# Optimization experiments

Measured on AMD Instinct MI355X. Metric: run time of the kernel, lower is better.

The kernel has to match this reference:

```python
import jax, jax.numpy as jnp
import numpy as np

B, L, H, ED, NCONV = 64, 2048, 128, 4, 3
N = B * L


def gat(x, src, dst, edge_attr, W, a_s, a_d, We, a_e, b, self_loops):
    """PyG GATConv, heads=1, concat=True, negative_slope=0.2, fill_value='mean'."""
    n = x.shape[0]
    h = x @ W                              # [N,H]
    a_src = h @ a_s                        # [N]
    a_dst = h @ a_d                        # [N]
    alpha = a_src[src] + a_dst[dst] + (edge_attr @ We) @ a_e  # [E]
    if self_loops:
        ones = jnp.ones(src.shape[0], x.dtype)
        deg = jax.ops.segment_sum(ones, dst, num_segments=n)
        mean_attr = jax.ops.segment_sum(edge_attr, dst, num_segments=n) / jnp.maximum(deg, 1.0)[:, None]
        loop_alpha = a_src + a_dst + (mean_attr @ We) @ a_e
        idx = jnp.arange(n, dtype=src.dtype)
        src = jnp.concatenate([src, idx])
        dst = jnp.concatenate([dst, idx])
        alpha = jnp.concatenate([alpha, loop_alpha])
    alpha = jax.nn.leaky_relu(alpha, 0.2)
    m = jax.ops.segment_max(alpha, dst, num_segments=n)
    ex = jnp.exp(alpha - m[dst])
    den = jax.ops.segment_sum(ex, dst, num_segments=n)
    coef = ex / jnp.maximum(den, 1e-16)[dst]
    return jax.ops.segment_sum(coef[:, None] * h[src], dst, num_segments=n) + b


def setup_inputs() -> dict:
    key = jax.random.key(0)
    ks = iter(jax.random.split(key, 32))
    # binary trees: per graph, node k>0 has parent (k-1)//2; edge child->parent (to_up)
    local = np.arange(1, L)
    parent = (local - 1) // 2
    offs = (np.arange(B) * L)[:, None]
    src = jnp.asarray((local[None, :] + offs).ravel(), dtype=jnp.int32)
    dst = jnp.asarray((parent[None, :] + offs).ravel(), dtype=jnp.int32)
    E = src.shape[0]
    s = 0.1
    inp = {
        "x": jax.random.normal(next(ks), (N,), jnp.float32),
        "src": src,
        "dst": dst,
        "edge_attr": jax.random.normal(next(ks), (E, ED), jnp.float32),
        "up_W0": jax.random.normal(next(ks), (1, H)) * s,
        "up_W": jax.random.normal(next(ks), (NCONV - 1, H, H)) * s,
        "up_att_src": jax.random.normal(next(ks), (NCONV, H)) * s,
        "up_att_dst": jax.random.normal(next(ks), (NCONV, H)) * s,
        "up_We": jax.random.normal(next(ks), (NCONV, ED, H)) * s,
        "up_att_edge": jax.random.normal(next(ks), (NCONV, H)) * s,
        "up_b": jax.random.normal(next(ks), (NCONV, H)) * s,
        "down_W": jax.random.normal(next(ks), (NCONV - 1, H, H)) * s,
        "down_att_src": jax.random.normal(next(ks), (NCONV - 1, H)) * s,
        "down_att_dst": jax.random.normal(next(ks), (NCONV - 1, H)) * s,
        "down_We": jax.random.normal(next(ks), (NCONV - 1, ED, H)) * s,
        "down_att_edge": jax.random.normal(next(ks), (NCONV - 1, H)) * s,
        "down_b": jax.random.normal(next(ks), (NCONV - 1, H)) * s,
        "lin_W": jax.random.normal(next(ks), (NCONV - 1, H, H)) * s,
        "lin_b": jax.random.normal(next(ks), (NCONV - 1, H)) * s,
        "lin_last_W": jax.random.normal(next(ks), (H, 1)) * s,
        "lin_last_b": jax.random.normal(next(ks), (1,)) * s,
    }
    return inp


def reference(x, src, dst, edge_attr, up_W0, up_W, up_att_src, up_att_dst, up_We,
              up_att_edge, up_b, down_W, down_att_src, down_att_dst, down_We,
              down_att_edge, down_b, lin_W, lin_b, lin_last_W, lin_last_b):
    h = x[:, None]                                            # flat_c.view(-1,1)
    # upward pass: toup GATConvs (with self loops) + relu
    for i in range(NCONV):
        W = up_W0 if i == 0 else up_W[i - 1]
        h = jax.nn.relu(gat(h, src, dst, edge_attr, W, up_att_src[i], up_att_dst[i],
                            up_We[i], up_att_edge[i], up_b[i], True))
    x_up = h
    # downward pass uses reversed edges, no self loops; replicates original's
    # indexing bug (todown[0] used twice, todown[-1] never used)
    src_d, dst_d = dst, src
    x_down = jax.nn.relu(gat(x_up, src_d, dst_d, edge_attr, down_W[0], down_att_src[0],
                             down_att_dst[0], down_We[0], down_att_edge[0], down_b[0], False))
    xx = x_down + x_up
    for i in range(NCONV - 1):
        xx = jax.nn.relu(xx @ lin_W[i] + lin_b[i])
        x_down = jax.nn.relu(gat(xx, src_d, dst_d, edge_attr, down_W[i], down_att_src[i],
                                 down_att_dst[i], down_We[i], down_att_edge[i], down_b[i], False))
        xx = x_down + x_up
    final_emb = xx
    out_nodes = xx @ lin_last_W + lin_last_b                  # [N,1]
    batch_out = out_nodes.reshape(B, L)                       # all graphs are max_len
    batch_emb = final_emb.reshape(B, L, H)
    out = batch_out - batch_out[:, :1]                        # subtract root node
    return out, batch_emb
```

## Files before the change

kernel.cpp:

```cpp
#include <hip/hip_runtime.h>
#include <hip/hip_bf16.h>
#include <cstdint>
#include <cstddef>

typedef unsigned short u16;
typedef short bf16x8 __attribute__((ext_vector_type(8)));
typedef float f32x4 __attribute__((ext_vector_type(4)));

#define Bn 64
#define Ln 2048
#define Hn 128
#define EDn 4
#define Nn (Bn*Ln)

#define CV_W0    0
#define CV_WUP   128
#define CV_AS    32896
#define CV_AD    33280
#define CV_WE    33664
#define CV_AE    35200
#define CV_BUP   35584
#define CV_WD    35968
#define CV_BD    68736
#define CV_WL    68992
#define CV_BL    101760
#define CV_WLAST 102016
#define CV_TOTAL 102144

__device__ __forceinline__ float b2f(u16 u) {
  union { float f; unsigned int i; } v; v.i = ((unsigned int)u) << 16; return v.f;
}
__device__ __forceinline__ u16 f2b(float f) {
  __hip_bfloat16 h = __float2bfloat16(f);
  union { __hip_bfloat16 h; u16 u; } v; v.h = h; return v.u;
}
__device__ __forceinline__ float lrelu(float v) { return v >= 0.f ? v : 0.2f * v; }
__device__ __forceinline__ float wave_sum(float r) {
  #pragma unroll
  for (int off = 32; off > 0; off >>= 1) r += __shfl_xor(r, off, 64);
  return r;
}
__device__ __forceinline__ float ld_in(const void* p, size_t i, int f) {
  return f ? b2f(((const u16*)p)[i]) : ((const float*)p)[i];
}
__device__ __forceinline__ u16* Cbase(void* dout, int f) {
  return f ? ((u16*)dout + Nn) : (u16*)((float*)dout + Nn);
}
__device__ __forceinline__ float lo16(unsigned v) { return b2f((u16)(v & 0xFFFF)); }
__device__ __forceinline__ float hi16(unsigned v) { return b2f((u16)(v >> 16)); }

__device__ __forceinline__ void gload_lds16(const void* g, void* l) {
  __builtin_amdgcn_global_load_lds(
      (const __attribute__((address_space(1))) void*)g,
      (__attribute__((address_space(3))) void*)l, 16, 0, 0);
}

__device__ __forceinline__ int xcd_remap(int bid, int nwg) {
  return (bid & 7) * (nwg >> 3) + (bid >> 3);
}

__global__ void detect_kernel(const u16* __restrict__ x, int* __restrict__ flag) {
  int lane = threadIdx.x;
  u16 u = x[lane];
  int e = (u >> 7) & 0xFF;
  bool good = (e >= 100 && e <= 140) || ((u & 0x7FFF) == 0);
  unsigned long long m = __ballot(good);
  if (lane == 0) *flag = (__popcll(m) >= 56) ? 1 : 0;
}

struct CvtArgs { const void* src[12]; int off[12]; int tr[12]; };
__global__ void cvt_kernel(CvtArgs a, const int* __restrict__ flagp, u16* __restrict__ dst) {
  int f = *flagp;
  int i = blockIdx.x * 256 + threadIdx.x;
  if (i >= CV_TOTAL) return;
  int s = 0;
  #pragma unroll
  for (int k = 1; k < 12; ++k) s = (i >= a.off[k]) ? k : s;
  int j = i - a.off[s];
  int sj = j;
  if (a.tr[s]) {
    int mat = j >> 14, jm = j & 16383;
    int r = jm >> 7, c = jm & 127;
    int us = c >> 3, sub = c & 7;
    int u = us ^ (r & 15);
    int k = u * 8 + sub;
    sj = (mat << 14) + k * 128 + r;
  }
  dst[i] = f ? ((const u16*)a.src[s])[sj] : f2b(((const float*)a.src[s])[sj]);
}

__global__ void up0_kernel(const void* __restrict__ x, const void* __restrict__ edge_attr,
                           const u16* __restrict__ W0, const u16* __restrict__ att_s,
                           const u16* __restrict__ att_d, const u16* __restrict__ We0,
                           const u16* __restrict__ ae0, const u16* __restrict__ b0,
                           u16* __restrict__ y, const int* __restrict__ flagp) {
  __shared__ float P[6];
  __shared__ float comb[64];
  __shared__ float W0s[Hn];
  __shared__ float b0s[Hn];
  int f = *flagp;
  int t = threadIdx.x;
  int lane = t & 63, w = t >> 6;
  if (w < 2) {
    const u16* vb = (w == 0) ? att_s : att_d;
    float r = b2f(W0[lane]) * b2f(vb[lane]) + b2f(W0[lane+64]) * b2f(vb[lane+64]);
    r = wave_sum(r);
    if (lane == 0) P[w] = r;
  } else {
    int e0 = (w - 2) * 2;
    float a0 = b2f(ae0[lane]), a1 = b2f(ae0[lane+64]);
    float r0 = b2f(We0[e0*Hn+lane])*a0     + b2f(We0[e0*Hn+lane+64])*a1;
    float r1 = b2f(We0[(e0+1)*Hn+lane])*a0 + b2f(We0[(e0+1)*Hn+lane+64])*a1;
    r0 = wave_sum(r0); r1 = wave_sum(r1);
    if (lane == 0) { P[2+e0] = r0; P[3+e0] = r1; }
  }
  if (t < Hn) { W0s[t] = b2f(W0[t]); b0s[t] = b2f(b0[t]); }
  __syncthreads();
  int base = xcd_remap(blockIdx.x, gridDim.x) * 64;
  if (t < 64) {
    int n = base + t;
    int local = n & (Ln - 1);
    int nb = n >> 11;
    int root = n - local;
    float S0 = P[0], D0 = P[1];
    float w0 = P[2], w1 = P[3], w2 = P[4], w3 = P[5];
    float xp = ld_in(x, n, f);
    float ad_p = D0 * xp;
    int c1l = 2*local + 1, c2l = 2*local + 2;
    int deg = (c1l < Ln ? 1 : 0) + (c2l < Ln ? 1 : 0);
    float e1 = 0.f, e2 = 0.f, xc1 = 0.f, xc2 = 0.f, sc1 = 0.f, sc2 = 0.f;
    if (deg >= 1) {
      xc1 = ld_in(x, root + c1l, f);
      size_t ei = ((size_t)nb*(Ln-1) + (c1l-1))*EDn;
      e1 = ld_in(edge_attr, ei+0, f)*w0 + ld_in(edge_attr, ei+1, f)*w1
         + ld_in(edge_attr, ei+2, f)*w2 + ld_in(edge_attr, ei+3, f)*w3;
      sc1 = lrelu(S0*xc1 + ad_p + e1);
    }
    if (deg == 2) {
      xc2 = ld_in(x, root + c2l, f);
      size_t ei = ((size_t)nb*(Ln-1) + (c2l-1))*EDn;
      e2 = ld_in(edge_attr, ei+0, f)*w0 + ld_in(edge_attr, ei+1, f)*w1
         + ld_in(edge_attr, ei+2, f)*w2 + ld_in(edge_attr, ei+3, f)*w3;
      sc2 = lrelu(S0*xc2 + ad_p + e2);
    }
    float mean_e = deg ? (e1 + e2) / (float)deg : 0.f;
    float ss = lrelu(S0*xp + ad_p + mean_e);
    float m = ss;
    if (deg >= 1) m = fmaxf(m, sc1);
    if (deg == 2) m = fmaxf(m, sc2);
    float es  = __expf(ss - m);
    float ec1 = (deg >= 1) ? __expf(sc1 - m) : 0.f;
    float ec2 = (deg == 2) ? __expf(sc2 - m) : 0.f;
    float den = es + ec1 + ec2;
    comb[t] = (es*xp + ec1*xc1 + ec2*xc2) / den;
  }
  __syncthreads();
  u16* out = y + (size_t)base * Hn;
  for (int i = t; i < 64*Hn/4; i += 256) {
    int row = i >> 5;
    int col = (i & 31) * 4;
    float c = comb[row];
    ushort4 st;
    st.x = f2b(fmaxf(c*W0s[col+0] + b0s[col+0], 0.f));
    st.y = f2b(fmaxf(c*W0s[col+1] + b0s[col+1], 0.f));
    st.z = f2b(fmaxf(c*W0s[col+2] + b0s[col+2], 0.f));
    st.w = f2b(fmaxf(c*W0s[col+3] + b0s[col+3], 0.f));
    *(ushort4*)&out[(size_t)i*4] = st;
  }
}

template<int GATHER, int EPI, int ASAD>
__global__ __launch_bounds__(256, 4) void gemm_k(
                       const u16* __restrict__ Xp, const u16* __restrict__ Wt,
                       const u16* __restrict__ bias, const u16* __restrict__ Uarr,
                       u16* __restrict__ outp, void* __restrict__ dout,
                       const int* __restrict__ flagp, int x_is_C, int out_mode,
                       float2* __restrict__ asad, const u16* __restrict__ avs,
                       const u16* __restrict__ avd, float* __restrict__ nodesp) {
  __shared__ u16 Ws[Hn*Hn];
  int f = *flagp;
  const u16* X = x_is_C ? Cbase(dout, f) : Xp;
  int t = threadIdx.x;
  int lane = t & 63, w = t >> 6;
  int m = lane & 15, q = lane >> 4;
  int row0 = xcd_remap(blockIdx.x, gridDim.x) * 128;
  int wbase = row0 + w*32;
  #pragma unroll
  for (int i = 0; i < 8; ++i)
    gload_lds16(Wt + (size_t)(i*256 + t)*8, &Ws[(size_t)(i*256 + (t & ~63))*8]);
  uint4 xf[2][4];
  #pragma unroll
  for (int rt = 0; rt < 2; ++rt) {
    int R = wbase + rt*16 + m;
    bool zero = false;
    const uint4* src;
    if (GATHER) {
      int local = R & (Ln - 1);
      if (local == 0) { zero = true; src = (const uint4*)X; }
      else src = (const uint4*)(X + (size_t)((R - local) + ((local - 1) >> 1))*Hn);
    } else {
      src = (const uint4*)(X + (size_t)R*Hn);
    }
    #pragma unroll
    for (int ki = 0; ki < 4; ++ki) {
      uint4 v = src[ki*4 + q];
      if (zero) { v.x = 0; v.y = 0; v.z = 0; v.w = 0; }
      xf[rt][ki] = v;
    }
  }
  __syncthreads();
  u16* Cb = Cbase(dout, f);
  float* emf = (float*)dout + Nn;
  u16* od = (out_mode == 0) ? outp : (out_mode == 1 ? Cb : (u16*)dout + Nn);
  float asv[2] = {0.f, 0.f}, adv[2] = {0.f, 0.f};
  #pragma unroll
  for (int cb = 0; cb < 2; ++cb) {
    f32x4 acc[2][4];
    #pragma unroll
    for (int rt = 0; rt < 2; ++rt)
      #pragma unroll
      for (int c4 = 0; c4 < 4; ++c4) acc[rt][c4] = (f32x4){0.f, 0.f, 0.f, 0.f};
    #pragma unroll
    for (int ki = 0; ki < 4; ++ki) {
      #pragma unroll
      for (int c4 = 0; c4 < 4; ++c4) {
        int ct = cb*4 + c4;
        bf16x8 wf = *(bf16x8*)&Ws[((ct*16 + m)*16 + ((ki*4 + q) ^ m))*8];
        #pragma unroll
        for (int rt = 0; rt < 2; ++rt)
          acc[rt][c4] = __builtin_amdgcn_mfma_f32_16x16x32_bf16(
                          wf, *(bf16x8*)&xf[rt][ki], acc[rt][c4], 0, 0, 0);
      }
    }
    #pragma unroll
    for (int rt = 0; rt < 2; ++rt) {
      int R = wbase + rt*16 + m;
      #pragma unroll
      for (int c4 = 0; c4 < 4; ++c4) {
        int ct = cb*4 + c4;
        int c0 = ct*16 + q*4;
        float o[4];
        #pragma unroll
        for (int r = 0; r < 4; ++r) o[r] = acc[rt][c4][r];
        if (ASAD == 1) {
          ushort4 sv = *(const ushort4*)&avs[c0];
          ushort4 dv = *(const ushort4*)&avd[c0];
          asv[rt] += o[0]*b2f(sv.x) + o[1]*b2f(sv.y) + o[2]*b2f(sv.z) + o[3]*b2f(sv.w);
          adv[rt] += o[0]*b2f(dv.x) + o[1]*b2f(dv.y) + o[2]*b2f(dv.z) + o[3]*b2f(dv.w);
        }
        if (EPI >= 1) {
          ushort4 bv = *(const ushort4*)&bias[c0];
          o[0] = fmaxf(o[0] + b2f(bv.x), 0.f); o[1] = fmaxf(o[1] + b2f(bv.y), 0.f);
          o[2] = fmaxf(o[2] + b2f(bv.z), 0.f); o[3] = fmaxf(o[3] + b2f(bv.w), 0.f);
        }
        if (EPI == 2) {
          ushort4 uv = *(const ushort4*)&Uarr[(size_t)R*Hn + c0];
          o[0] += b2f(uv.x); o[1] += b2f(uv.y); o[2] += b2f(uv.z); o[3] += b2f(uv.w);
        }
        if (ASAD == 2) {
          ushort4 sv = *(const ushort4*)&avs[c0];
          asv[rt] += o[0]*b2f(sv.x) + o[1]*b2f(sv.y) + o[2]*b2f(sv.z) + o[3]*b2f(sv.w);
        }
        if (out_mode == 2 && !f) {
          float4 fv; fv.x = o[0]; fv.y = o[1]; fv.z = o[2]; fv.w = o[3];
          *(float4*)&emf[(size_t)R*Hn + c0] = fv;
        } else {
          ushort4 st; st.x = f2b(o[0]); st.y = f2b(o[1]); st.z = f2b(o[2]); st.w = f2b(o[3]);
          *(ushort4*)&od[(size_t)R*Hn + c0] = st;
        }
      }
    }
  }
  #pragma unroll
  for (int rt = 0; rt < 2; ++rt) {
    int R = wbase + rt*16 + m;
    if (ASAD == 1) {
      float as_ = asv[rt], ad_ = adv[rt];
      as_ += __shfl_xor(as_, 16, 64); as_ += __shfl_xor(as_, 32, 64);
      ad_ += __shfl_xor(ad_, 16, 64); ad_ += __shfl_xor(ad_, 32, 64);
      if (q == 0) { float2 v; v.x = as_; v.y = ad_; asad[R] = v; }
    }
    if (ASAD == 2) {
      float as_ = asv[rt];
      as_ += __shfl_xor(as_, 16, 64); as_ += __shfl_xor(as_, 32, 64);
      if (q == 0) nodesp[R] = as_;
    }
  }
}

__global__ __launch_bounds__(256, 4) void gemm_blend_k(
                       const u16* __restrict__ Wt, const float2* __restrict__ coef,
                       const u16* __restrict__ bias_up, u16* __restrict__ outp,
                       void* __restrict__ dout, const int* __restrict__ flagp,
                       float2* __restrict__ asad, const u16* __restrict__ avs,
                       const u16* __restrict__ avd) {
  __shared__ u16 Ws[Hn*Hn];
  int f = *flagp;
  const u16* h = Cbase(dout, f);
  int t = threadIdx.x;
  int lane = t & 63, w = t >> 6;
  int m = lane & 15, q = lane >> 4;
  int row0 = xcd_remap(blockIdx.x, gridDim.x) * 128;
  int wbase = row0 + w*32;
  #pragma unroll
  for (int i = 0; i < 8; ++i)
    gload_lds16(Wt + (size_t)(i*256 + t)*8, &Ws[(size_t)(i*256 + (t & ~63))*8]);
  uint4 xf[2][4];
  #pragma unroll
  for (int rt = 0; rt < 2; ++rt) {
    int R = wbase + rt*16 + m;
    int local = R & (Ln - 1);
    int root = R - local;
    int c1l = 2*local + 1, c2l = 2*local + 2;
    int r1 = (c1l < Ln) ? root + c1l : R;
    int r2 = (c2l < Ln) ? root + c2l : R;
    float2 cf = coef[R];
    float es = 1.f - cf.x - cf.y;
    const uint4* hp = (const uint4*)(h + (size_t)R*Hn);
    const uint4* h1 = (const uint4*)(h + (size_t)r1*Hn);
    const uint4* h2 = (const uint4*)(h + (size_t)r2*Hn);
    #pragma unroll
    for (int ki = 0; ki < 4; ++ki) {
      int u = ki*4 + q;
      uint4 a = hp[u], b = h1[u], c = h2[u];
      uint4 bv = ((const uint4*)bias_up)[u];
      uint4 st;
      #pragma unroll
      for (int i = 0; i < 4; ++i) {
        unsigned av = ((unsigned*)&a)[i], b1v = ((unsigned*)&b)[i];
        unsigned b2v = ((unsigned*)&c)[i], bbv = ((unsigned*)&bv)[i];
        float o0 = es*lo16(av) + cf.x*lo16(b1v) + cf.y*lo16(b2v) + lo16(bbv);
        float o1 = es*hi16(av) + cf.x*hi16(b1v) + cf.y*hi16(b2v) + hi16(bbv);
        ((unsigned*)&st)[i] = (unsigned)f2b(fmaxf(o0, 0.f))
                            | ((unsigned)f2b(fmaxf(o1, 0.f)) << 16);
      }
      xf[rt][ki] = st;
    }
  }
  __syncthreads();
  float asv[2] = {0.f, 0.f}, adv[2] = {0.f, 0.f};
  #pragma unroll
  for (int cb = 0; cb < 2; ++cb) {
    f32x4 acc[2][4];
    #pragma unroll
    for (int rt = 0; rt < 2; ++rt)
      #pragma unroll
      for (int c4 = 0; c4 < 4; ++c4) acc[rt][c4] = (f32x4){0.f, 0.f, 0.f, 0.f};
    #pragma unroll
    for (int ki = 0; ki < 4; ++ki) {
      #pragma unroll
      for (int c4 = 0; c4 < 4; ++c4) {
        int ct = cb*4 + c4;
        bf16x8 wf = *(bf16x8*)&Ws[((ct*16 + m)*16 + ((ki*4 + q) ^ m))*8];
        #pragma unroll
        for (int rt = 0; rt < 2; ++rt)
          acc[rt][c4] = __builtin_amdgcn_mfma_f32_16x16x32_bf16(
                          wf, *(bf16x8*)&xf[rt][ki], acc[rt][c4], 0, 0, 0);
      }
    }
    #pragma unroll
    for (int rt = 0; rt < 2; ++rt) {
      int R = wbase + rt*16 + m;
      #pragma unroll
      for (int c4 = 0; c4 < 4; ++c4) {
        int ct = cb*4 + c4;
        int c0 = ct*16 + q*4;
        float o0 = acc[rt][c4][0], o1 = acc[rt][c4][1];
        float o2 = acc[rt][c4][2], o3 = acc[rt][c4][3];
        ushort4 sv = *(const ushort4*)&avs[c0];
        ushort4 dv = *(const ushort4*)&avd[c0];
        asv[rt] += o0*b2f(sv.x) + o1*b2f(sv.y) + o2*b2f(sv.z) + o3*b2f(sv.w);
        adv[rt] += o0*b2f(dv.x) + o1*b2f(dv.y) + o2*b2f(dv.z) + o3*b2f(dv.w);
        ushort4 st; st.x = f2b(o0); st.y = f2b(o1); st.z = f2b(o2); st.w = f2b(o3);
        *(ushort4*)&outp[(size_t)R*Hn + c0] = st;
      }
    }
  }
  #pragma unroll
  for (int rt = 0; rt < 2; ++rt) {
    int R = wbase + rt*16 + m;
    float as_ = asv[rt], ad_ = adv[rt];
    as_ += __shfl_xor(as_, 16, 64); as_ += __shfl_xor(as_, 32, 64);
    ad_ += __shfl_xor(ad_, 16, 64); ad_ += __shfl_xor(ad_, 32, 64);
    if (q == 0) { float2 v; v.x = as_; v.y = ad_; asad[R] = v; }
  }
}

__global__ __launch_bounds__(512, 4) void fused_down_lin_k(
                       const u16* __restrict__ Xp, const u16* __restrict__ Wdt,
                       const u16* __restrict__ bd, const u16* __restrict__ Uarr,
                       const u16* __restrict__ Wlt, const u16* __restrict__ bl,
                       u16* __restrict__ outp) {
  __shared__ u16 Ws[Hn*Hn];
  __shared__ u16 XX[128*Hn];
  int t = threadIdx.x;
  int lane = t & 63, w = t >> 6;
  int m = lane & 15, q = lane >> 4;
  int row0 = xcd_remap(blockIdx.x, gridDim.x) * 128;
  int R = row0 + w*16 + m;
  int rl = w*16 + m;
  #pragma unroll
  for (int i = 0; i < 4; ++i)
    gload_lds16(Wdt + (size_t)(i*512 + t)*8, &Ws[(size_t)(i*512 + (t & ~63))*8]);
  uint4 xf[4];
  {
    int local = R & (Ln - 1);
    bool zero = (local == 0);
    const uint4* src = zero ? (const uint4*)Xp
                     : (const uint4*)(Xp + (size_t)((R - local) + ((local - 1) >> 1))*Hn);
    #pragma unroll
    for (int ki = 0; ki < 4; ++ki) {
      uint4 v = src[ki*4 + q];
      if (zero) { v.x = 0; v.y = 0; v.z = 0; v.w = 0; }
      xf[ki] = v;
    }
  }
  __syncthreads();
  f32x4 acc[8];
  #pragma unroll
  for (int ct = 0; ct < 8; ++ct) acc[ct] = (f32x4){0.f, 0.f, 0.f, 0.f};
  #pragma unroll
  for (int ki = 0; ki < 4; ++ki) {
    #pragma unroll
    for (int ct = 0; ct < 8; ++ct) {
      bf16x8 wf = *(bf16x8*)&Ws[((ct*16 + m)*16 + ((ki*4 + q) ^ m))*8];
      acc[ct] = __builtin_amdgcn_mfma_f32_16x16x32_bf16(
                    wf, *(bf16x8*)&xf[ki], acc[ct], 0, 0, 0);
    }
  }
  __syncthreads();
  #pragma unroll
  for (int i = 0; i < 4; ++i)
    gload_lds16(Wlt + (size_t)(i*512 + t)*8, &Ws[(size_t)(i*512 + (t & ~63))*8]);
  #pragma unroll
  for (int ct = 0; ct < 8; ++ct) {
    int c0 = ct*16 + q*4;
    ushort4 bv = *(const ushort4*)&bd[c0];
    ushort4 uv = *(const ushort4*)&Uarr[(size_t)R*Hn + c0];
    float o0 = fmaxf(acc[ct][0] + b2f(bv.x), 0.f) + b2f(uv.x);
    float o1 = fmaxf(acc[ct][1] + b2f(bv.y), 0.f) + b2f(uv.y);
    float o2 = fmaxf(acc[ct][2] + b2f(bv.z), 0.f) + b2f(uv.z);
    float o3 = fmaxf(acc[ct][3] + b2f(bv.w), 0.f) + b2f(uv.w);
    int uu = (2*ct + (q >> 1)) ^ m;
    uint2 pk;
    pk.x = (unsigned)f2b(o0) | ((unsigned)f2b(o1) << 16);
    pk.y = (unsigned)f2b(o2) | ((unsigned)f2b(o3) << 16);
    *(uint2*)&XX[rl*Hn + uu*8 + (q & 1)*4] = pk;
  }
  __syncthreads();
  f32x4 acc2[8];
  #pragma unroll
  for (int ct = 0; ct < 8; ++ct) acc2[ct] = (f32x4){0.f, 0.f, 0.f, 0.f};
  #pragma unroll
  for (int ki = 0; ki < 4; ++ki) {
    #pragma unroll
    for (int ct = 0; ct < 8; ++ct) {
      bf16x8 wf = *(bf16x8*)&Ws[((ct*16 + m)*16 + ((ki*4 + q) ^ m))*8];
      bf16x8 xb = *(bf16x8*)&XX[rl*Hn + (((ki*4 + q) ^ m))*8];
      acc2[ct] = __builtin_amdgcn_mfma_f32_16x16x32_bf16(wf, xb, acc2[ct], 0, 0, 0);
    }
  }
  #pragma unroll
  for (int ct = 0; ct < 8; ++ct) {
    int c0 = ct*16 + q*4;
    ushort4 bv = *(const ushort4*)&bl[c0];
    ushort4 st;
    st.x = f2b(fmaxf(acc2[ct][0] + b2f(bv.x), 0.f));
    st.y = f2b(fmaxf(acc2[ct][1] + b2f(bv.y), 0.f));
    st.z = f2b(fmaxf(acc2[ct][2] + b2f(bv.z), 0.f));
    st.w = f2b(fmaxf(acc2[ct][3] + b2f(bv.w), 0.f));
    *(ushort4*)&outp[(size_t)R*Hn + c0] = st;
  }
}

__global__ void coef_kernel(const void* __restrict__ edge_attr,
                            const u16* __restrict__ We, const u16* __restrict__ ae,
                            const float2* __restrict__ asad, float2* __restrict__ coef,
                            const int* __restrict__ flagp) {
  __shared__ float P[4];
  int f = *flagp;
  int t = threadIdx.x;
  int lane = t & 63, w = t >> 6;
  {
    unsigned av = *(const unsigned*)&ae[2*lane];
    unsigned wv = *(const unsigned*)&We[w*Hn + 2*lane];
    float r = wave_sum(lo16(wv)*lo16(av) + hi16(wv)*hi16(av));
    if (lane == 0) P[w] = r;
  }
  __syncthreads();
  int p = xcd_remap(blockIdx.x, gridDim.x) * 256 + t;
  int local = p & (Ln - 1);
  int root = p - local;
  int nb = p >> 11;
  int c1l = 2*local + 1, c2l = 2*local + 2;
  int deg = (c1l < Ln ? 1 : 0) + (c2l < Ln ? 1 : 0);
  float2 aa = asad[p];
  float w0 = P[0], w1 = P[1], w2 = P[2], w3 = P[3];
  float e1 = 0.f, e2 = 0.f, sc1 = 0.f, sc2 = 0.f;
  if (deg >= 1) {
    size_t ei = ((size_t)nb*(Ln-1) + (c1l-1))*EDn;
    if (f) {
      ushort4 v = *(const ushort4*)((const u16*)edge_attr + ei);
      e1 = b2f(v.x)*w0 + b2f(v.y)*w1 + b2f(v.z)*w2 + b2f(v.w)*w3;
      if (deg == 2) {
        ushort4 v2 = *(const ushort4*)((const u16*)edge_attr + ei + EDn);
        e2 = b2f(v2.x)*w0 + b2f(v2.y)*w1 + b2f(v2.z)*w2 + b2f(v2.w)*w3;
      }
    } else {
      float4 v = *(const float4*)((const float*)edge_attr + ei);
      e1 = v.x*w0 + v.y*w1 + v.z*w2 + v.w*w3;
      if (deg == 2) {
        float4 v2 = *(const float4*)((const float*)edge_attr + ei + EDn);
        e2 = v2.x*w0 + v2.y*w1 + v2.z*w2 + v2.w*w3;
      }
    }
    sc1 = lrelu(asad[root + c1l].x + aa.y + e1);
    if (deg == 2) sc2 = lrelu(asad[root + c2l].x + aa.y + e2);
  }
  float mean_e = deg ? (e1 + e2) / (float)deg : 0.f;
  float ss = lrelu(aa.x + aa.y + mean_e);
  float m = ss;
  if (deg >= 1) m = fmaxf(m, sc1);
  if (deg == 2) m = fmaxf(m, sc2);
  float es  = __expf(ss - m);
  float ec1 = (deg >= 1) ? __expf(sc1 - m) : 0.f;
  float ec2 = (deg == 2) ? __expf(sc2 - m) : 0.f;
  float inv = 1.f / (es + ec1 + ec2);
  float2 cf; cf.x = ec1 * inv; cf.y = ec2 * inv;
  coef[p] = cf;
}

__global__ void blend_kernel(const u16* __restrict__ h, const float2* __restrict__ coef,
                             const u16* __restrict__ bias, u16* __restrict__ y) {
  int t = threadIdx.x;
  int g = t & 15;
  int p = xcd_remap(blockIdx.x, gridDim.x) * 16 + (t >> 4);
  int local = p & (Ln - 1);
  int root = p - local;
  int c1l = 2*local + 1, c2l = 2*local + 2;
  int deg = (c1l < Ln ? 1 : 0) + (c2l < Ln ? 1 : 0);
  float2 cf = coef[p];
  float es = 1.f - cf.x - cf.y;
  int off = g * 8;
  uint4 hp = *(const uint4*)&h[(size_t)p*Hn + off];
  uint4 h1 = {0,0,0,0}, h2 = {0,0,0,0};
  if (deg >= 1) h1 = *(const uint4*)&h[(size_t)(root + c1l)*Hn + off];
  if (deg == 2) h2 = *(const uint4*)&h[(size_t)(root + c2l)*Hn + off];
  uint4 bv = *(const uint4*)&bias[off];
  uint4 st;
  #pragma unroll
  for (int i = 0; i < 4; ++i) {
    unsigned a = ((unsigned*)&hp)[i], b1 = ((unsigned*)&h1)[i];
    unsigned b2 = ((unsigned*)&h2)[i], bb = ((unsigned*)&bv)[i];
    float o0 = es*lo16(a) + cf.x*lo16(b1) + cf.y*lo16(b2) + lo16(bb);
    float o1 = es*hi16(a) + cf.x*hi16(b1) + cf.y*hi16(b2) + hi16(bb);
    ((unsigned*)&st)[i] = (unsigned)f2b(fmaxf(o0, 0.f)) | ((unsigned)f2b(fmaxf(o1, 0.f)) << 16);
  }
  *(uint4*)&y[(size_t)p*Hn + off] = st;
}

__global__ void score_kernel(const float* __restrict__ nodes, void* __restrict__ dout,
                             const int* __restrict__ flagp) {
  int f = *flagp;
  int n = xcd_remap(blockIdx.x, gridDim.x) * 256 + threadIdx.x;
  float v = nodes[n] - nodes[n & ~(Ln - 1)];
  if (f) ((u16*)dout)[n] = f2b(v);
  else   ((float*)dout)[n] = v;
}

extern "C" void kernel_launch(void* const* d_in, const int* in_sizes, int n_in,
                              void* d_out, int out_size, void* d_ws, size_t ws_size,
                              hipStream_t stream) {
  const void* x         = d_in[0];
  const void* edge_attr = d_in[3];

  u16* Ubuf = (u16*)d_ws;
  u16* Abuf = Ubuf + (size_t)Nn*Hn;
  u16* Bbuf = Abuf + (size_t)Nn*Hn;
  u16* cvt  = Bbuf + (size_t)Nn*Hn;
  float2* asad = (float2*)(cvt + CV_TOTAL);
  float2* coef = asad + Nn;
  float* nodes = (float*)(coef + Nn);
  int* flag = (int*)(nodes + Nn);

  detect_kernel<<<1, 64, 0, stream>>>((const u16*)d_in[0], flag);

  CvtArgs ca;
  ca.src[0]  = d_in[4];  ca.off[0]  = CV_W0;    ca.tr[0]  = 0;
  ca.src[1]  = d_in[5];  ca.off[1]  = CV_WUP;   ca.tr[1]  = 1;
  ca.src[2]  = d_in[6];  ca.off[2]  = CV_AS;    ca.tr[2]  = 0;
  ca.src[3]  = d_in[7];  ca.off[3]  = CV_AD;    ca.tr[3]  = 0;
  ca.src[4]  = d_in[8];  ca.off[4]  = CV_WE;    ca.tr[4]  = 0;
  ca.src[5]  = d_in[9];  ca.off[5]  = CV_AE;    ca.tr[5]  = 0;
  ca.src[6]  = d_in[10]; ca.off[6]  = CV_BUP;   ca.tr[6]  = 0;
  ca.src[7]  = d_in[11]; ca.off[7]  = CV_WD;    ca.tr[7]  = 1;
  ca.src[8]  = d_in[16]; ca.off[8]  = CV_BD;    ca.tr[8]  = 0;
  ca.src[9]  = d_in[17]; ca.off[9]  = CV_WL;    ca.tr[9]  = 1;
  ca.src[10] = d_in[18]; ca.off[10] = CV_BL;    ca.tr[10] = 0;
  ca.src[11] = d_in[19]; ca.off[11] = CV_WLAST; ca.tr[11] = 0;
  cvt_kernel<<<(CV_TOTAL + 255)/256, 256, 0, stream>>>(ca, flag, cvt);

  up0_kernel<<<Nn/64, 256, 0, stream>>>(x, edge_attr, cvt+CV_W0, cvt+CV_AS, cvt+CV_AD,
                                        cvt+CV_WE, cvt+CV_AE, cvt+CV_BUP, Abuf, flag);
  gemm_k<0,0,1><<<Nn/128, 256, 0, stream>>>(Abuf, cvt+CV_WUP, nullptr, nullptr,
                                         nullptr, d_out, flag, 0, 1,
                                         asad, cvt+CV_AS+Hn, cvt+CV_AD+Hn, nullptr);
  coef_kernel<<<Nn/256, 256, 0, stream>>>(edge_attr, cvt+CV_WE+EDn*Hn, cvt+CV_AE+Hn,
                                          asad, coef, flag);
  gemm_blend_k<<<Nn/128, 256, 0, stream>>>(cvt+CV_WUP+Hn*Hn, coef, cvt+CV_BUP+Hn,
                                           Bbuf, d_out, flag,
                                           asad, cvt+CV_AS+2*Hn, cvt+CV_AD+2*Hn);
  coef_kernel<<<Nn/256, 256, 0, stream>>>(edge_attr, cvt+CV_WE+2*EDn*Hn, cvt+CV_AE+2*Hn,
                                          asad, coef, flag);
  blend_kernel<<<Nn/16, 256, 0, stream>>>(Bbuf, coef, cvt+CV_BUP+2*Hn, Ubuf);

  fused_down_lin_k<<<Nn/128, 512, 0, stream>>>(Ubuf, cvt+CV_WD, cvt+CV_BD, Ubuf,
                                               cvt+CV_WL, cvt+CV_BL, Abuf);
  fused_down_lin_k<<<Nn/128, 512, 0, stream>>>(Abuf, cvt+CV_WD, cvt+CV_BD, Ubuf,
                                               cvt+CV_WL+Hn*Hn, cvt+CV_BL+Hn, Bbuf);
  gemm_k<1,2,2><<<Nn/128, 256, 0, stream>>>(Bbuf, cvt+CV_WD+Hn*Hn, cvt+CV_BD+Hn, Ubuf,
                                         nullptr, d_out, flag, 0, 2,
                                         nullptr, cvt+CV_WLAST, nullptr, nodes);

  score_kernel<<<Nn/256, 256, 0, stream>>>(nodes, d_out, flag);
}
```

Baseline: 277.5 us.

## Fuse attention coefficient computation into blend kernels and double rows per gemm block

The two coef_kernel launches are removed; each consumer (gemm_blend_k, blend_kernel) recomputes softmax coefficients inline from asad and edge_attr, with the small edge-weight dot products precomputed once by a new prep_kernel. gemm_k now processes 256 rows per block, loading the weight tile into LDS once and prefetching the second row tile while the first is computed, with launch bounds lowered to 3. A separate asad2 buffer avoids a read/write hazard on asad. This removes launches and the coef round-trip, at the cost of redundant coefficient math per thread, higher register pressure and half as many gemm blocks.

```diff
diff --git a/kernel.cpp b/kernel.cpp
--- a/kernel.cpp
+++ b/kernel.cpp
@@ -59,6 +59,49 @@
   return (bid & 7) * (nwg >> 3) + (bid >> 3);
 }
 
+__device__ __forceinline__ float2 coef_row(int p, const float2* __restrict__ asr,
+                                           const void* __restrict__ edge_attr, int f,
+                                           float w0, float w1, float w2, float w3) {
+  int local = p & (Ln - 1);
+  int root = p - local;
+  int nb = p >> 11;
+  int c1l = 2*local + 1, c2l = 2*local + 2;
+  int deg = (c1l < Ln ? 1 : 0) + (c2l < Ln ? 1 : 0);
+  float2 aa = asr[p];
+  float e1 = 0.f, e2 = 0.f, sc1 = 0.f, sc2 = 0.f;
+  if (deg >= 1) {
+    size_t ei = ((size_t)nb*(Ln-1) + (c1l-1))*EDn;
+    if (f) {
+      ushort4 v = *(const ushort4*)((const u16*)edge_attr + ei);
+      e1 = b2f(v.x)*w0 + b2f(v.y)*w1 + b2f(v.z)*w2 + b2f(v.w)*w3;
+      if (deg == 2) {
+        ushort4 v2 = *(const ushort4*)((const u16*)edge_attr + ei + EDn);
+        e2 = b2f(v2.x)*w0 + b2f(v2.y)*w1 + b2f(v2.z)*w2 + b2f(v2.w)*w3;
+      }
+    } else {
+      float4 v = *(const float4*)((const float*)edge_attr + ei);
+      e1 = v.x*w0 + v.y*w1 + v.z*w2 + v.w*w3;
+      if (deg == 2) {
+        float4 v2 = *(const float4*)((const float*)edge_attr + ei + EDn);
+        e2 = v2.x*w0 + v2.y*w1 + v2.z*w2 + v2.w*w3;
+      }
+    }
+    sc1 = lrelu(asr[root + c1l].x + aa.y + e1);
+    if (deg == 2) sc2 = lrelu(asr[root + c2l].x + aa.y + e2);
+  }
+  float mean_e = deg ? (e1 + e2) / (float)deg : 0.f;
+  float ss = lrelu(aa.x + aa.y + mean_e);
+  float m = ss;
+  if (deg >= 1) m = fmaxf(m, sc1);
+  if (deg == 2) m = fmaxf(m, sc2);
+  float es  = __expf(ss - m);
+  float ec1 = (deg >= 1) ? __expf(sc1 - m) : 0.f;
+  float ec2 = (deg == 2) ? __expf(sc2 - m) : 0.f;
+  float inv = 1.f / (es + ec1 + ec2);
+  float2 cf; cf.x = ec1 * inv; cf.y = ec2 * inv;
+  return cf;
+}
+
 __global__ void detect_kernel(const u16* __restrict__ x, int* __restrict__ flag) {
   int lane = threadIdx.x;
   u16 u = x[lane];
@@ -89,41 +132,39 @@
   dst[i] = f ? ((const u16*)a.src[s])[sj] : f2b(((const float*)a.src[s])[sj]);
 }
 
+__global__ void prep_kernel(const u16* __restrict__ cvt, float* __restrict__ P) {
+  int lane = threadIdx.x & 63;
+  #pragma unroll
+  for (int d = 0; d < 14; ++d) {
+    int ao, bo;
+    if (d == 0)      { ao = CV_W0; bo = CV_AS; }
+    else if (d == 1) { ao = CV_W0; bo = CV_AD; }
+    else { int i = (d-2) >> 2, e = (d-2) & 3; ao = CV_WE + i*EDn*Hn + e*Hn; bo = CV_AE + i*Hn; }
+    float r = b2f(cvt[ao+lane])*b2f(cvt[bo+lane])
+            + b2f(cvt[ao+lane+64])*b2f(cvt[bo+lane+64]);
+    r = wave_sum(r);
+    if (lane == 0) P[d] = r;
+  }
+}
+
 __global__ void up0_kernel(const void* __restrict__ x, const void* __restrict__ edge_attr,
-                           const u16* __restrict__ W0, const u16* __restrict__ att_s,
-                           const u16* __restrict__ att_d, const u16* __restrict__ We0,
-                           const u16* __restrict__ ae0, const u16* __restrict__ b0,
+                           const u16* __restrict__ W0, const u16* __restrict__ b0,
+                           const float* __restrict__ Pd,
                            u16* __restrict__ y, const int* __restrict__ flagp) {
-  __shared__ float P[6];
   __shared__ float comb[64];
   __shared__ float W0s[Hn];
   __shared__ float b0s[Hn];
   int f = *flagp;
   int t = threadIdx.x;
-  int lane = t & 63, w = t >> 6;
-  if (w < 2) {
-    const u16* vb = (w == 0) ? att_s : att_d;
-    float r = b2f(W0[lane]) * b2f(vb[lane]) + b2f(W0[lane+64]) * b2f(vb[lane+64]);
-    r = wave_sum(r);
-    if (lane == 0) P[w] = r;
-  } else {
-    int e0 = (w - 2) * 2;
-    float a0 = b2f(ae0[lane]), a1 = b2f(ae0[lane+64]);
-    float r0 = b2f(We0[e0*Hn+lane])*a0     + b2f(We0[e0*Hn+lane+64])*a1;
-    float r1 = b2f(We0[(e0+1)*Hn+lane])*a0 + b2f(We0[(e0+1)*Hn+lane+64])*a1;
-    r0 = wave_sum(r0); r1 = wave_sum(r1);
-    if (lane == 0) { P[2+e0] = r0; P[3+e0] = r1; }
-  }
   if (t < Hn) { W0s[t] = b2f(W0[t]); b0s[t] = b2f(b0[t]); }
-  __syncthreads();
   int base = xcd_remap(blockIdx.x, gridDim.x) * 64;
   if (t < 64) {
     int n = base + t;
     int local = n & (Ln - 1);
     int nb = n >> 11;
     int root = n - local;
-    float S0 = P[0], D0 = P[1];
-    float w0 = P[2], w1 = P[3], w2 = P[4], w3 = P[5];
+    float S0 = Pd[0], D0 = Pd[1];
+    float w0 = Pd[2], w1 = Pd[3], w2 = Pd[4], w3 = Pd[5];
     float xp = ld_in(x, n, f);
     float ad_p = D0 * xp;
     int c1l = 2*local + 1, c2l = 2*local + 2;
@@ -169,26 +210,9 @@
   }
 }
 
-template<int GATHER, int EPI, int ASAD>
-__global__ __launch_bounds__(256, 4) void gemm_k(
-                       const u16* __restrict__ Xp, const u16* __restrict__ Wt,
-                       const u16* __restrict__ bias, const u16* __restrict__ Uarr,
-                       u16* __restrict__ outp, void* __restrict__ dout,
-                       const int* __restrict__ flagp, int x_is_C, int out_mode,
-                       float2* __restrict__ asad, const u16* __restrict__ avs,
-                       const u16* __restrict__ avd, float* __restrict__ nodesp) {
-  __shared__ u16 Ws[Hn*Hn];
-  int f = *flagp;
-  const u16* X = x_is_C ? Cbase(dout, f) : Xp;
-  int t = threadIdx.x;
-  int lane = t & 63, w = t >> 6;
-  int m = lane & 15, q = lane >> 4;
-  int row0 = xcd_remap(blockIdx.x, gridDim.x) * 128;
-  int wbase = row0 + w*32;
-  #pragma unroll
-  for (int i = 0; i < 8; ++i)
-    gload_lds16(Wt + (size_t)(i*256 + t)*8, &Ws[(size_t)(i*256 + (t & ~63))*8]);
-  uint4 xf[2][4];
+template<int GATHER>
+__device__ __forceinline__ void load_x(uint4 (&xf)[2][4], const u16* __restrict__ X,
+                                       int wbase, int m, int q) {
   #pragma unroll
   for (int rt = 0; rt < 2; ++rt) {
     int R = wbase + rt*16 + m;
@@ -208,10 +232,15 @@
       xf[rt][ki] = v;
     }
   }
-  __syncthreads();
-  u16* Cb = Cbase(dout, f);
-  float* emf = (float*)dout + Nn;
-  u16* od = (out_mode == 0) ? outp : (out_mode == 1 ? Cb : (u16*)dout + Nn);
+}
+
+template<int EPI, int ASAD>
+__device__ __forceinline__ void compute_tile(
+    const uint4 (&xf)[2][4], const u16* Ws, int wbase, int m, int q, int f,
+    const u16* __restrict__ bias, const u16* __restrict__ Uarr,
+    u16* __restrict__ od, float* __restrict__ emf, int out_mode,
+    float2* __restrict__ asad, const u16* __restrict__ avs,
+    const u16* __restrict__ avd, float* __restrict__ nodesp) {
   float asv[2] = {0.f, 0.f}, adv[2] = {0.f, 0.f};
   #pragma unroll
   for (int cb = 0; cb < 2; ++cb) {
@@ -288,11 +317,46 @@
   }
 }
 
+template<int GATHER, int EPI, int ASAD>
+__global__ __launch_bounds__(256, 3) void gemm_k(
+                       const u16* __restrict__ Xp, const u16* __restrict__ Wt,
+                       const u16* __restrict__ bias, const u16* __restrict__ Uarr,
+                       u16* __restrict__ outp, void* __restrict__ dout,
+                       const int* __restrict__ flagp, int x_is_C, int out_mode,
+                       float2* __restrict__ asad, const u16* __restrict__ avs,
+                       const u16* __restrict__ avd, float* __restrict__ nodesp) {
+  __shared__ u16 Ws[Hn*Hn];
+  int f = *flagp;
+  const u16* X = x_is_C ? Cbase(dout, f) : Xp;
+  int t = threadIdx.x;
+  int lane = t & 63, w = t >> 6;
+  int m = lane & 15, q = lane >> 4;
+  int row0 = xcd_remap(blockIdx.x, gridDim.x) * 256;
+  int wb0 = row0 + w*32;
+  int wb1 = row0 + 128 + w*32;
+  #pragma unroll
+  for (int i = 0; i < 8; ++i)
+    gload_lds16(Wt + (size_t)(i*256 + t)*8, &Ws[(size_t)(i*256 + (t & ~63))*8]);
+  uint4 xf0[2][4];
+  load_x<GATHER>(xf0, X, wb0, m, q);
+  __syncthreads();
+  uint4 xf1[2][4];
+  load_x<GATHER>(xf1, X, wb1, m, q);
+  u16* Cb = Cbase(dout, f);
+  float* emf = (float*)dout + Nn;
+  u16* od = (out_mode == 0) ? outp : (out_mode == 1 ? Cb : (u16*)dout + Nn);
+  compute_tile<EPI, ASAD>(xf0, Ws, wb0, m, q, f, bias, Uarr, od, emf, out_mode,
+                          asad, avs, avd, nodesp);
+  compute_tile<EPI, ASAD>(xf1, Ws, wb1, m, q, f, bias, Uarr, od, emf, out_mode,
+                          asad, avs, avd, nodesp);
+}
+
 __global__ __launch_bounds__(256, 4) void gemm_blend_k(
-                       const u16* __restrict__ Wt, const float2* __restrict__ coef,
+                       const u16* __restrict__ Wt, const void* __restrict__ edge_attr,
+                       const float2* __restrict__ asad_in, const float* __restrict__ Pd,
                        const u16* __restrict__ bias_up, u16* __restrict__ outp,
                        void* __restrict__ dout, const int* __restrict__ flagp,
-                       float2* __restrict__ asad, const u16* __restrict__ avs,
+                       float2* __restrict__ asad2, const u16* __restrict__ avs,
                        const u16* __restrict__ avd) {
   __shared__ u16 Ws[Hn*Hn];
   int f = *flagp;
@@ -302,6 +366,7 @@
   int m = lane & 15, q = lane >> 4;
   int row0 = xcd_remap(blockIdx.x, gridDim.x) * 128;
   int wbase = row0 + w*32;
+  float we0 = Pd[6], we1 = Pd[7], we2 = Pd[8], we3 = Pd[9];
   #pragma unroll
   for (int i = 0; i < 8; ++i)
     gload_lds16(Wt + (size_t)(i*256 + t)*8, &Ws[(size_t)(i*256 + (t & ~63))*8]);
@@ -314,7 +379,7 @@
     int c1l = 2*local + 1, c2l = 2*local + 2;
     int r1 = (c1l < Ln) ? root + c1l : R;
     int r2 = (c2l < Ln) ? root + c2l : R;
-    float2 cf = coef[R];
+    float2 cf = coef_row(R, asad_in, edge_attr, f, we0, we1, we2, we3);
     float es = 1.f - cf.x - cf.y;
     const uint4* hp = (const uint4*)(h + (size_t)R*Hn);
     const uint4* h1 = (const uint4*)(h + (size_t)r1*Hn);
@@ -382,7 +447,7 @@
     float as_ = asv[rt], ad_ = adv[rt];
     as_ += __shfl_xor(as_, 16, 64); as_ += __shfl_xor(as_, 32, 64);
     ad_ += __shfl_xor(ad_, 16, 64); ad_ += __shfl_xor(ad_, 32, 64);
-    if (q == 0) { float2 v; v.x = as_; v.y = ad_; asad[R] = v; }
+    if (q == 0) { float2 v; v.x = as_; v.y = ad_; asad2[R] = v; }
   }
 }
 
@@ -473,65 +538,11 @@
   }
 }
 
-__global__ void coef_kernel(const void* __restrict__ edge_attr,
-                            const u16* __restrict__ We, const u16* __restrict__ ae,
-                            const float2* __restrict__ asad, float2* __restrict__ coef,
-                            const int* __restrict__ flagp) {
-  __shared__ float P[4];
+__global__ void blend_kernel(const u16* __restrict__ h, const void* __restrict__ edge_attr,
+                             const float2* __restrict__ asad2, const float* __restrict__ Pd,
+                             const u16* __restrict__ bias, u16* __restrict__ y,
+                             const int* __restrict__ flagp) {
   int f = *flagp;
-  int t = threadIdx.x;
-  int lane = t & 63, w = t >> 6;
-  {
-    unsigned av = *(const unsigned*)&ae[2*lane];
-    unsigned wv = *(const unsigned*)&We[w*Hn + 2*lane];
-    float r = wave_sum(lo16(wv)*lo16(av) + hi16(wv)*hi16(av));
-    if (lane == 0) P[w] = r;
-  }
-  __syncthreads();
-  int p = xcd_remap(blockIdx.x, gridDim.x) * 256 + t;
-  int local = p & (Ln - 1);
-  int root = p - local;
-  int nb = p >> 11;
-  int c1l = 2*local + 1, c2l = 2*local + 2;
-  int deg = (c1l < Ln ? 1 : 0) + (c2l < Ln ? 1 : 0);
-  float2 aa = asad[p];
-  float w0 = P[0], w1 = P[1], w2 = P[2], w3 = P[3];
-  float e1 = 0.f, e2 = 0.f, sc1 = 0.f, sc2 = 0.f;
-  if (deg >= 1) {
-    size_t ei = ((size_t)nb*(Ln-1) + (c1l-1))*EDn;
-    if (f) {
-      ushort4 v = *(const ushort4*)((const u16*)edge_attr + ei);
-      e1 = b2f(v.x)*w0 + b2f(v.y)*w1 + b2f(v.z)*w2 + b2f(v.w)*w3;
-      if (deg == 2) {
-        ushort4 v2 = *(const ushort4*)((const u16*)edge_attr + ei + EDn);
-        e2 = b2f(v2.x)*w0 + b2f(v2.y)*w1 + b2f(v2.z)*w2 + b2f(v2.w)*w3;
-      }
-    } else {
-      float4 v = *(const float4*)((const float*)edge_attr + ei);
-      e1 = v.x*w0 + v.y*w1 + v.z*w2 + v.w*w3;
-      if (deg == 2) {
-        float4 v2 = *(const float4*)((const float*)edge_attr + ei + EDn);
-        e2 = v2.x*w0 + v2.y*w1 + v2.z*w2 + v2.w*w3;
-      }
-    }
-    sc1 = lrelu(asad[root + c1l].x + aa.y + e1);
-    if (deg == 2) sc2 = lrelu(asad[root + c2l].x + aa.y + e2);
-  }
-  float mean_e = deg ? (e1 + e2) / (float)deg : 0.f;
-  float ss = lrelu(aa.x + aa.y + mean_e);
-  float m = ss;
-  if (deg >= 1) m = fmaxf(m, sc1);
-  if (deg == 2) m = fmaxf(m, sc2);
-  float es  = __expf(ss - m);
-  float ec1 = (deg >= 1) ? __expf(sc1 - m) : 0.f;
-  float ec2 = (deg == 2) ? __expf(sc2 - m) : 0.f;
-  float inv = 1.f / (es + ec1 + ec2);
-  float2 cf; cf.x = ec1 * inv; cf.y = ec2 * inv;
-  coef[p] = cf;
-}
-
-__global__ void blend_kernel(const u16* __restrict__ h, const float2* __restrict__ coef,
-                             const u16* __restrict__ bias, u16* __restrict__ y) {
   int t = threadIdx.x;
   int g = t & 15;
   int p = xcd_remap(blockIdx.x, gridDim.x) * 16 + (t >> 4);
@@ -539,7 +550,7 @@
   int root = p - local;
   int c1l = 2*local + 1, c2l = 2*local + 2;
   int deg = (c1l < Ln ? 1 : 0) + (c2l < Ln ? 1 : 0);
-  float2 cf = coef[p];
+  float2 cf = coef_row(p, asad2, edge_attr, f, Pd[10], Pd[11], Pd[12], Pd[13]);
   float es = 1.f - cf.x - cf.y;
   int off = g * 8;
   uint4 hp = *(const uint4*)&h[(size_t)p*Hn + off];
@@ -578,10 +589,11 @@
   u16* Abuf = Ubuf + (size_t)Nn*Hn;
   u16* Bbuf = Abuf + (size_t)Nn*Hn;
   u16* cvt  = Bbuf + (size_t)Nn*Hn;
-  float2* asad = (float2*)(cvt + CV_TOTAL);
-  float2* coef = asad + Nn;
-  float* nodes = (float*)(coef + Nn);
+  float2* asad  = (float2*)(cvt + CV_TOTAL);
+  float2* asad2 = asad + Nn;
+  float* nodes = (float*)(asad2 + Nn);
   int* flag = (int*)(nodes + Nn);
+  float* Pdots = (float*)(flag + 4);
 
   detect_kernel<<<1, 64, 0, stream>>>((const u16*)d_in[0], flag);
 
@@ -599,26 +611,24 @@
   ca.src[10] = d_in[18]; ca.off[10] = CV_BL;    ca.tr[10] = 0;
   ca.src[11] = d_in[19]; ca.off[11] = CV_WLAST; ca.tr[11] = 0;
   cvt_kernel<<<(CV_TOTAL + 255)/256, 256, 0, stream>>>(ca, flag, cvt);
-
-  up0_kernel<<<Nn/64, 256, 0, stream>>>(x, edge_attr, cvt+CV_W0, cvt+CV_AS, cvt+CV_AD,
-                                        cvt+CV_WE, cvt+CV_AE, cvt+CV_BUP, Abuf, flag);
-  gemm_k<0,0,1><<<Nn/128, 256, 0, stream>>>(Abuf, cvt+CV_WUP, nullptr, nullptr,
+  prep_kernel<<<1, 64, 0, stream>>>(cvt, Pdots);
+
+  up0_kernel<<<Nn/64, 256, 0, stream>>>(x, edge_attr, cvt+CV_W0, cvt+CV_BUP,
+                                        Pdots, Abuf, flag);
+  gemm_k<0,0,1><<<Nn/256, 256, 0, stream>>>(Abuf, cvt+CV_WUP, nullptr, nullptr,
                                          nullptr, d_out, flag, 0, 1,
                                          asad, cvt+CV_AS+Hn, cvt+CV_AD+Hn, nullptr);
-  coef_kernel<<<Nn/256, 256, 0, stream>>>(edge_attr, cvt+CV_WE+EDn*Hn, cvt+CV_AE+Hn,
-                                          asad, coef, flag);
-  gemm_blend_k<<<Nn/128, 256, 0, stream>>>(cvt+CV_WUP+Hn*Hn, coef, cvt+CV_BUP+Hn,
-                                           Bbuf, d_out, flag,
-                                           asad, cvt+CV_AS+2*Hn, cvt+CV_AD+2*Hn);
-  coef_kernel<<<Nn/256, 256, 0, stream>>>(edge_attr, cvt+CV_WE+2*EDn*Hn, cvt+CV_AE+2*Hn,
-                                          asad, coef, flag);
-  blend_kernel<<<Nn/16, 256, 0, stream>>>(Bbuf, coef, cvt+CV_BUP+2*Hn, Ubuf);
+  gemm_blend_k<<<Nn/128, 256, 0, stream>>>(cvt+CV_WUP+Hn*Hn, edge_attr, asad, Pdots,
+                                           cvt+CV_BUP+Hn, Bbuf, d_out, flag,
+                                           asad2, cvt+CV_AS+2*Hn, cvt+CV_AD+2*Hn);
+  blend_kernel<<<Nn/16, 256, 0, stream>>>(Bbuf, edge_attr, asad2, Pdots,
+                                          cvt+CV_BUP+2*Hn, Ubuf, flag);
 
   fused_down_lin_k<<<Nn/128, 512, 0, stream>>>(Ubuf, cvt+CV_WD, cvt+CV_BD, Ubuf,
                                                cvt+CV_WL, cvt+CV_BL, Abuf);
   fused_down_lin_k<<<Nn/128, 512, 0, stream>>>(Abuf, cvt+CV_WD, cvt+CV_BD, Ubuf,
                                                cvt+CV_WL+Hn*Hn, cvt+CV_BL+Hn, Bbuf);
-  gemm_k<1,2,2><<<Nn/128, 256, 0, stream>>>(Bbuf, cvt+CV_WD+Hn*Hn, cvt+CV_BD+Hn, Ubuf,
+  gemm_k<1,2,2><<<Nn/256, 256, 0, stream>>>(Bbuf, cvt+CV_WD+Hn*Hn, cvt+CV_BD+Hn, Ubuf,
                                          nullptr, d_out, flag, 0, 2,
                                          nullptr, cvt+CV_WLAST, nullptr, nodes);
 
```

New measurement: 279.5 us. Within noise of the previous version (+0.7%).
